# Kernel tuning notes

Measured on AMD Instinct MI355X. Metric: run time of the kernel, lower is better.

## Reference

```python
import jax, jax.numpy as jnp
import numpy as np

# Module hyperparams (from init_kwargs)
B, C, F, K, H, W = 8, 32, 32, 3, 32, 32
Q = K * K          # kernel positions
PAD = K // 2       # 'same' padding (output spatial == input spatial)
# groups = in_channels (num_groups=None default) -> step = 1, weight axis = F*Q*C


def setup_inputs() -> dict:
    key = jax.random.key(0)
    k1, k2, k3 = jax.random.split(key, 3)
    x = jax.random.normal(k1, (B, C, H, W), dtype=jnp.float32)
    # learned per-weight rational coefficients: one rational per (f, kernel_pos, channel)
    nums = jax.random.normal(k2, (F * Q * C, 6), dtype=jnp.float32) * 0.1
    denoms = jax.random.normal(k3, (F * Q * C, 4), dtype=jnp.float32) * 0.1
    return {"x": x, "nums": nums, "denoms": denoms}


def reference(x, nums, denoms):
    # per-weight Pade rational activation over conv windows, scatter-accumulated
    # into output channels:
    #   out[b,f,y,x] = sum_{q in KxK, c} P_{f,q,c}(w) / (1 + |D_{f,q,c}(w)|),
    #   w = zero-padded input at window position q, channel c.
    a = nums.reshape(F, Q, C, 6)    # numerator coeffs, powers 0..5
    b = denoms.reshape(F, Q, C, 4)  # denominator coeffs, powers 1..4

    xp = jnp.pad(x, ((0, 0), (0, 0), (PAD, PAD), (PAD, PAD)))
    # gather K*K shifted views: [B, C, Q, H, W]
    win = jnp.stack([xp[:, :, i:i + H, j:j + W]
                     for i in range(K) for j in range(K)], axis=2)

    # powers w^0..w^5: [B, C, Q, 6, H, W]
    w1 = win
    w2 = w1 * w1
    w3 = w2 * w1
    w4 = w2 * w2
    w5 = w4 * w1
    pows = jnp.stack([jnp.ones_like(w1), w1, w2, w3, w4, w5], axis=3)

    # numerator P and denominator D, per (f, q, c): [B, F, Q, C, H, W]
    num = jnp.einsum('bcqphw,fqcp->bfqchw', pows, a)
    den = 1.0 + jnp.abs(jnp.einsum('bcqphw,fqcp->bfqchw', pows[:, :, :, 1:5], b))

    # accumulate over kernel positions and channels -> [B, F, H, W]
    return jnp.sum(num / den, axis=(2, 3))
```

## Files before the change

### kernel.cpp

```cpp
#include <hip/hip_runtime.h>
#include <math.h>

#define NB 8
#define NC 32
#define NF 32
#define NH 32
#define NW 32
#define NQ 9
#define CSPLIT 4
#define CPB (NC / CSPLIT)
#define TROWS 18
#define TS 34
#define TILE_N (TROWS * TS)

__global__ __launch_bounds__(256, 8) void ka_conv_rational_kernel(
    const float* __restrict__ x,
    const float* __restrict__ nums,
    const float* __restrict__ dens,
    float* __restrict__ out)
{
    __shared__ float tile[2][TILE_N];

    const int t    = threadIdx.x;
    const int bid  = blockIdx.x;
    const int cs   = bid & (CSPLIT - 1);
    const int half = (bid >> 2) & 1;
    const int bf   = bid >> 3;
    const int f    = bf & (NF - 1);
    const int bb   = bf >> 5;
    const int xx   = t & 31;
    const int ty   = t >> 5;
    const int c0   = cs * CPB;

    int  soff[3];
    bool svalid[3];
#pragma unroll
    for (int i = 0; i < 3; ++i) {
        int idx = t + i * 256;
        int ry  = idx / TS;
        int rx  = idx - ry * TS;
        int gy  = half * 16 + ry - 1;
        int gx  = rx - 1;
        bool ok = (idx < TILE_N) && (gy >= 0) && (gy < NH) && (gx >= 0) && (gx < NW);
        svalid[i] = ok;
        soff[i]   = ok ? (gy * NW + gx) : 0;
    }

    const float* __restrict__ xb    = x    + ((size_t)bb * NC + c0) * NH * NW;
    const float* __restrict__ abase = nums + (size_t)f * NQ * NC * 6;
    const float* __restrict__ bbase = dens + (size_t)f * NQ * NC * 4;

    float st[3];
#pragma unroll
    for (int i = 0; i < 3; ++i)
        st[i] = xb[soff[i]];

    float acc0 = 0.f, acc1 = 0.f;

    for (int ci = 0; ci < CPB; ++ci) {
        const int c = c0 + ci;
        float* tl = tile[ci & 1];

#pragma unroll
        for (int i = 0; i < 3; ++i) {
            int idx = t + i * 256;
            if (idx < TILE_N)
                tl[idx] = svalid[i] ? st[i] : 0.f;
        }
        if (ci + 1 < CPB) {
            const float* xc = xb + (size_t)(ci + 1) * NH * NW;
#pragma unroll
            for (int i = 0; i < 3; ++i)
                st[i] = xc[soff[i]];
        }
        __syncthreads();

        float n[4][3];
#pragma unroll
        for (int dy = 0; dy < 4; ++dy)
#pragma unroll
            for (int dx = 0; dx < 3; ++dx)
                n[dy][dx] = tl[(ty * 2 + dy) * TS + (xx + dx)];

#pragma unroll
        for (int q = 0; q < NQ; ++q) {
            const float* ap = abase + (size_t)(q * NC + c) * 6;
            const float* bp = bbase + (size_t)(q * NC + c) * 4;
            const float a0 = ap[0], a1 = ap[1], a2 = ap[2],
                        a3 = ap[3], a4 = ap[4], a5 = ap[5];
            const float d0 = bp[0], d1 = bp[1], d2 = bp[2], d3 = bp[3];
            const int qi = q / 3, qj = q - qi * 3;

            {
                const float w  = n[qi][qj];
                float nu = fmaf(fmaf(fmaf(fmaf(fmaf(a5, w, a4), w, a3), w, a2), w, a1), w, a0);
                float dp = fmaf(fmaf(fmaf(d3, w, d2), w, d1), w, d0) * w;
                float de = 1.0f + fabsf(dp);
                acc0 = fmaf(nu, __builtin_amdgcn_rcpf(de), acc0);
            }
            {
                const float w  = n[qi + 1][qj];
                float nu = fmaf(fmaf(fmaf(fmaf(fmaf(a5, w, a4), w, a3), w, a2), w, a1), w, a0);
                float dp = fmaf(fmaf(fmaf(d3, w, d2), w, d1), w, d0) * w;
                float de = 1.0f + fabsf(dp);
                acc1 = fmaf(nu, __builtin_amdgcn_rcpf(de), acc1);
            }
        }
    }

    const int y0 = half * 16 + ty * 2;
    float* op = out + ((size_t)bf * NH + y0) * NW + xx;
    unsafeAtomicAdd(op, acc0);
    unsafeAtomicAdd(op + NW, acc1);
}

extern "C" void kernel_launch(void* const* d_in, const int* in_sizes, int n_in,
                              void* d_out, int out_size, void* d_ws, size_t ws_size,
                              hipStream_t stream) {
    const float* x    = (const float*)d_in[0];
    const float* nums = (const float*)d_in[1];
    const float* dens = (const float*)d_in[2];
    float* out = (float*)d_out;

    hipMemsetAsync(d_out, 0, (size_t)out_size * sizeof(float), stream);

    dim3 grid(NB * NF * 2 * CSPLIT);
    dim3 block(256);
    ka_conv_rational_kernel<<<grid, block, 0, stream>>>(x, nums, dens, out);
}
```

Baseline: 85.41 us.

## Prepad input and repack coefficients into workspace; drop shared-memory tile

Adds two pre-kernels: one packs the numerator and denominator coefficients into aligned 12-float records, and one writes a zero-padded copy of x (34x36 per channel) into the workspace. The main kernel then reads each thread's 4x4 window straight from global memory as float4 vectors with register double-buffering, which removes the LDS tile, the __syncthreads and the boundary checks. Coefficient loads become contiguous per record and can be vectorised. The cost is two extra kernel launches and extra global traffic for the padded copy and the repacked coefficients, and every thread now issues its own unaligned vector global loads.

```diff
diff --git a/kernel.cpp b/kernel.cpp
--- a/kernel.cpp
+++ b/kernel.cpp
@@ -9,18 +9,49 @@
 #define NQ 9
 #define CSPLIT 4
 #define CPB (NC / CSPLIT)
-#define TROWS 18
-#define TS 34
-#define TILE_N (TROWS * TS)
+
+#define PROWS 34
+#define PCOLS 36
+
+#define NREC (NF * NQ * NC)
+#define COEFF_FLOATS (NREC * 12)
+#define XPAD_FLOATS (NB * NC * PROWS * PCOLS)
+
+typedef float f4 __attribute__((ext_vector_type(4), aligned(4)));
+
+__global__ __launch_bounds__(256) void reformat_coeffs(
+    const float* __restrict__ nums, const float* __restrict__ dens,
+    float* __restrict__ rec)
+{
+    int r = blockIdx.x * 256 + threadIdx.x;
+    if (r >= NREC) return;
+    const float* a = nums + (size_t)r * 6;
+    const float* d = dens + (size_t)r * 4;
+    float* o = rec + (size_t)r * 12;
+    o[0] = a[0]; o[1] = a[1]; o[2]  = a[2]; o[3]  = a[3];
+    o[4] = d[0]; o[5] = d[1]; o[6]  = d[2]; o[7]  = d[3];
+    o[8] = a[4]; o[9] = a[5]; o[10] = 0.f;  o[11] = 0.f;
+}
+
+__global__ __launch_bounds__(256) void prepad_x(
+    const float* __restrict__ x, float* __restrict__ xp)
+{
+    int idx = blockIdx.x * 256 + threadIdx.x;
+    int px  = idx % PCOLS;
+    int t1  = idx / PCOLS;
+    int py  = t1 % PROWS;
+    int bc  = t1 / PROWS;
+    float v = 0.f;
+    if (py >= 1 && py <= NH && px >= 1 && px <= NW)
+        v = x[(size_t)bc * NH * NW + (py - 1) * NW + (px - 1)];
+    xp[idx] = v;
+}
 
 __global__ __launch_bounds__(256, 8) void ka_conv_rational_kernel(
-    const float* __restrict__ x,
-    const float* __restrict__ nums,
-    const float* __restrict__ dens,
+    const float* __restrict__ cf,
+    const float* __restrict__ xp,
     float* __restrict__ out)
 {
-    __shared__ float tile[2][TILE_N];
-
     const int t    = threadIdx.x;
     const int bid  = blockIdx.x;
     const int cs   = bid & (CSPLIT - 1);
@@ -30,87 +61,58 @@
     const int bb   = bf >> 5;
     const int xx   = t & 31;
     const int ty   = t >> 5;
+    const int y0   = half * 16 + ty * 2;
     const int c0   = cs * CPB;
 
-    int  soff[3];
-    bool svalid[3];
+    const float* xbase = xp + (((size_t)(bb * NC + c0) * PROWS) + y0) * PCOLS + xx;
+    const float* cfb   = cf + (size_t)(f * NQ * NC + c0) * 12;
+
+    f4 cur[4], nxt[4];
 #pragma unroll
-    for (int i = 0; i < 3; ++i) {
-        int idx = t + i * 256;
-        int ry  = idx / TS;
-        int rx  = idx - ry * TS;
-        int gy  = half * 16 + ry - 1;
-        int gx  = rx - 1;
-        bool ok = (idx < TILE_N) && (gy >= 0) && (gy < NH) && (gx >= 0) && (gx < NW);
-        svalid[i] = ok;
-        soff[i]   = ok ? (gy * NW + gx) : 0;
-    }
-
-    const float* __restrict__ xb    = x    + ((size_t)bb * NC + c0) * NH * NW;
-    const float* __restrict__ abase = nums + (size_t)f * NQ * NC * 6;
-    const float* __restrict__ bbase = dens + (size_t)f * NQ * NC * 4;
-
-    float st[3];
-#pragma unroll
-    for (int i = 0; i < 3; ++i)
-        st[i] = xb[soff[i]];
+    for (int r = 0; r < 4; ++r)
+        cur[r] = *(const f4*)(xbase + r * PCOLS);
 
     float acc0 = 0.f, acc1 = 0.f;
 
     for (int ci = 0; ci < CPB; ++ci) {
-        const int c = c0 + ci;
-        float* tl = tile[ci & 1];
-
+        if (ci + 1 < CPB) {
+            const float* xn = xbase + (size_t)(ci + 1) * PROWS * PCOLS;
 #pragma unroll
-        for (int i = 0; i < 3; ++i) {
-            int idx = t + i * 256;
-            if (idx < TILE_N)
-                tl[idx] = svalid[i] ? st[i] : 0.f;
+            for (int r = 0; r < 4; ++r)
+                nxt[r] = *(const f4*)(xn + r * PCOLS);
         }
-        if (ci + 1 < CPB) {
-            const float* xc = xb + (size_t)(ci + 1) * NH * NW;
-#pragma unroll
-            for (int i = 0; i < 3; ++i)
-                st[i] = xc[soff[i]];
-        }
-        __syncthreads();
-
-        float n[4][3];
-#pragma unroll
-        for (int dy = 0; dy < 4; ++dy)
-#pragma unroll
-            for (int dx = 0; dx < 3; ++dx)
-                n[dy][dx] = tl[(ty * 2 + dy) * TS + (xx + dx)];
 
 #pragma unroll
         for (int q = 0; q < NQ; ++q) {
-            const float* ap = abase + (size_t)(q * NC + c) * 6;
-            const float* bp = bbase + (size_t)(q * NC + c) * 4;
-            const float a0 = ap[0], a1 = ap[1], a2 = ap[2],
-                        a3 = ap[3], a4 = ap[4], a5 = ap[5];
-            const float d0 = bp[0], d1 = bp[1], d2 = bp[2], d3 = bp[3];
+            const float* rp = cfb + (size_t)(q * NC + ci) * 12;
+            const float a0 = rp[0], a1 = rp[1], a2 = rp[2], a3 = rp[3];
+            const float d0 = rp[4], d1 = rp[5], d2 = rp[6], d3 = rp[7];
+            const float a4 = rp[8], a5 = rp[9];
             const int qi = q / 3, qj = q - qi * 3;
 
             {
-                const float w  = n[qi][qj];
+                const float w  = cur[qi][qj];
                 float nu = fmaf(fmaf(fmaf(fmaf(fmaf(a5, w, a4), w, a3), w, a2), w, a1), w, a0);
                 float dp = fmaf(fmaf(fmaf(d3, w, d2), w, d1), w, d0) * w;
                 float de = 1.0f + fabsf(dp);
                 acc0 = fmaf(nu, __builtin_amdgcn_rcpf(de), acc0);
             }
             {
-                const float w  = n[qi + 1][qj];
+                const float w  = cur[qi + 1][qj];
                 float nu = fmaf(fmaf(fmaf(fmaf(fmaf(a5, w, a4), w, a3), w, a2), w, a1), w, a0);
                 float dp = fmaf(fmaf(fmaf(d3, w, d2), w, d1), w, d0) * w;
                 float de = 1.0f + fabsf(dp);
                 acc1 = fmaf(nu, __builtin_amdgcn_rcpf(de), acc1);
             }
         }
+
+#pragma unroll
+        for (int r = 0; r < 4; ++r)
+            cur[r] = nxt[r];
     }
 
-    const int y0 = half * 16 + ty * 2;
     float* op = out + ((size_t)bf * NH + y0) * NW + xx;
-    unsafeAtomicAdd(op, acc0);
+    unsafeAtomicAdd(op,      acc0);
     unsafeAtomicAdd(op + NW, acc1);
 }
 
@@ -122,9 +124,14 @@
     const float* dens = (const float*)d_in[2];
     float* out = (float*)d_out;
 
+    float* cf = (float*)d_ws;
+    float* xpad = cf + COEFF_FLOATS;
+
+    reformat_coeffs<<<(NREC + 255) / 256, 256, 0, stream>>>(nums, dens, cf);
+    prepad_x<<<XPAD_FLOATS / 256, 256, 0, stream>>>(x, xpad);
+
     hipMemsetAsync(d_out, 0, (size_t)out_size * sizeof(float), stream);
 
     dim3 grid(NB * NF * 2 * CSPLIT);
-    dim3 block(256);
-    ka_conv_rational_kernel<<<grid, block, 0, stream>>>(x, nums, dens, out);
+    ka_conv_rational_kernel<<<grid, 256, 0, stream>>>(cf, xpad, out);
 }
```

New measurement: 88.24 us. +3.3%, slower.
